# Kernel optimization log

Hardware: AMD Instinct MI355X
Metric: run time of the kernel (lower is better)

Reference implementation:

```python
import jax, jax.numpy as jnp
import numpy as np

N = 50000      # nodes
E = 800000     # edges (before self-loops)
F_IN = 256     # num_features
H = 8          # heads (conv1)
C = 32         # hidden_size per head (conv1)
OUT = 2        # conv2 out channels (1 head)
NEG_SLOPE = 0.2


def setup_inputs() -> dict:
    key = jax.random.key(0)
    ks = jax.random.split(key, 12)
    x = jax.random.normal(ks[0], (N, F_IN), jnp.float32)
    edge_index = jax.random.randint(ks[1], (2, E), 0, N, dtype=jnp.int64)

    def glorot(k, shape):
        fan = shape[0] if len(shape) == 2 else int(np.prod(shape))
        s = float(np.sqrt(6.0 / (fan + shape[-1])))
        return jax.random.uniform(k, shape, jnp.float32, -s, s)

    W1 = glorot(ks[2], (F_IN, H * C))
    att_src1 = glorot(ks[3], (H, C))
    att_dst1 = glorot(ks[4], (H, C))
    b1 = jnp.zeros((H * C,), jnp.float32)
    W2 = glorot(ks[5], (H * C, 1 * OUT))
    att_src2 = glorot(ks[6], (1, OUT))
    att_dst2 = glorot(ks[7], (1, OUT))
    b2 = jnp.zeros((OUT,), jnp.float32)
    return {"x": x, "edge_index": edge_index, "W1": W1, "att_src1": att_src1,
            "att_dst1": att_dst1, "b1": b1, "W2": W2, "att_src2": att_src2,
            "att_dst2": att_dst2, "b2": b2}


def gat_conv(x, src, dst, W, a_src, a_dst, b, heads, ch, n):
    # x: [n, f] -> projected [n, heads, ch]
    xp = (x @ W).reshape(n, heads, ch)
    alpha_src = jnp.einsum('nhc,hc->nh', xp, a_src)   # [n, H]
    alpha_dst = jnp.einsum('nhc,hc->nh', xp, a_dst)   # [n, H]
    e = jax.nn.leaky_relu(alpha_src[src] + alpha_dst[dst], NEG_SLOPE)  # [E', H]
    # segment softmax over edges grouped by destination node
    m = jax.ops.segment_max(e, dst, num_segments=n)                    # [n, H]
    p = jnp.exp(e - m[dst])
    denom = jax.ops.segment_sum(p, dst, num_segments=n)                # [n, H]
    alpha = p / denom[dst]                                             # [E', H]
    # weighted scatter-aggregate of source messages
    out = jax.ops.segment_sum(xp[src] * alpha[:, :, None], dst, num_segments=n)
    return out.reshape(n, heads * ch) + b


def reference(x, edge_index, W1, att_src1, att_dst1, b1, W2, att_src2, att_dst2, b2):
    n = x.shape[0]
    loops = jnp.arange(n, dtype=edge_index.dtype)  # GATConv add_self_loops=True
    src = jnp.concatenate([edge_index[0], loops])
    dst = jnp.concatenate([edge_index[1], loops])
    h = jax.nn.relu(gat_conv(x, src, dst, W1, att_src1, att_dst1, b1, H, C, n))
    # eval mode: F.dropout and attention dropout are identity
    return gat_conv(h, src, dst, W2, att_src2, att_dst2, b2, 1, OUT, n)
```

## Files before the change

kernel.cpp:

```cpp
#include <hip/hip_runtime.h>
#include <math.h>

#define N_NODES 50000
#define N_EDGES 800000
#define EP (N_EDGES + N_NODES)
#define NEG 0.2f
#define SCAN_BLOCKS 49
#define HB N_NODES

typedef __attribute__((ext_vector_type(8))) short bf16x8;
typedef __attribute__((ext_vector_type(4))) float f32x4;
typedef __attribute__((ext_vector_type(2))) float f32x2;

static __device__ __forceinline__ unsigned short bf16_rn(float f) {
    union { float f; unsigned int u; } v; v.f = f;
    unsigned int u = v.u;
    unsigned int r = (u + 0x7FFFu + ((u >> 16) & 1u)) >> 16;
    return (unsigned short)r;
}
static __device__ __forceinline__ f32x2 bf2_unpack(unsigned int u) {
    union { unsigned int i; float f; } a, b;
    a.i = u << 16; b.i = u & 0xFFFF0000u;
    return (f32x2){a.f, b.f};
}


__global__ void k_hist(const int* __restrict__ ei, int* __restrict__ counts) {
    int e = blockIdx.x * 256 + threadIdx.x;
    if (e >= EP) return;
    int d = (e < N_EDGES) ? ei[N_EDGES + e] : (e - N_EDGES);
    atomicAdd(&counts[d], 1);
}

__global__ void k_scan_block(const int* __restrict__ counts, int* __restrict__ excl,
                             int* __restrict__ bsums) {
    __shared__ int wsum[4];
    int b = blockIdx.x, t = threadIdx.x;
    int lane = t & 63, w = t >> 6;
    int i0 = b * 1024 + t * 4;
    int v0 = (i0 + 0 < N_NODES) ? counts[i0 + 0] : 0;
    int v1 = (i0 + 1 < N_NODES) ? counts[i0 + 1] : 0;
    int v2 = (i0 + 2 < N_NODES) ? counts[i0 + 2] : 0;
    int v3 = (i0 + 3 < N_NODES) ? counts[i0 + 3] : 0;
    int s = v0 + v1 + v2 + v3;
    int incl = s;
    #pragma unroll
    for (int d = 1; d < 64; d <<= 1) {
        int u = __shfl_up(incl, d);
        if (lane >= d) incl += u;
    }
    if (lane == 63) wsum[w] = incl;
    __syncthreads();
    if (t == 0) {
        int run = 0;
        #pragma unroll
        for (int i = 0; i < 4; ++i) { int x = wsum[i]; wsum[i] = run; run += x; }
        bsums[b] = run;
    }
    __syncthreads();
    int base = wsum[w] + incl - s;
    if (i0 + 0 < N_NODES) excl[i0 + 0] = base;
    if (i0 + 1 < N_NODES) excl[i0 + 1] = base + v0;
    if (i0 + 2 < N_NODES) excl[i0 + 2] = base + v0 + v1;
    if (i0 + 3 < N_NODES) excl[i0 + 3] = base + v0 + v1 + v2;
}

__global__ void k_scan_add(int* __restrict__ row_ptr, const int* __restrict__ bsums) {
    __shared__ int soff;
    int b = blockIdx.x, t = threadIdx.x;
    if (t < 64) {
        int v = (t < SCAN_BLOCKS) ? bsums[t] : 0;
        int incl = v;
        #pragma unroll
        for (int d = 1; d < 64; d <<= 1) {
            int u = __shfl_up(incl, d);
            if (t >= d) incl += u;
        }
        if (t == b) soff = incl - v;
    }
    __syncthreads();
    int off = soff;
    int i0 = b * 1024 + t * 4;
    #pragma unroll
    for (int j = 0; j < 4; ++j)
        if (i0 + j < N_NODES) row_ptr[i0 + j] += off;
    if (b == 0 && t == 0) row_ptr[N_NODES] = EP;
}

__global__ void k_scatter(const int* __restrict__ ei, const int* __restrict__ row_ptr,
                          int* __restrict__ fill, int* __restrict__ colb) {
    int e = blockIdx.x * 256 + threadIdx.x;
    if (e >= EP) return;
    int s, d;
    if (e < N_EDGES) { s = ei[e]; d = ei[N_EDGES + e]; }
    else             { s = e - N_EDGES; d = s; }
    int pos = row_ptr[d] + atomicAdd(&fill[d], 1);
    colb[pos] = s;
}

__global__ void k_cvtWfrag(const float* __restrict__ W1, bf16x8* __restrict__ Wfrag) {
    int ft = blockIdx.x * 256 + threadIdx.x;
    int c = ft >> 10, rem = ft & 1023;
    int nt = rem >> 6, l = rem & 63;
    int n = (l & 15) * 16 + nt;
    int k0 = c * 32 + (l >> 4) * 8;
    bf16x8 f;
    #pragma unroll
    for (int j = 0; j < 8; ++j)
        f[j] = (short)bf16_rn(W1[(k0 + j) * 256 + n]);
    Wfrag[ft] = f;
}

#define GM_GRID 782
__global__ __launch_bounds__(256) void
k_gemm1m(const float* __restrict__ x, const bf16x8* __restrict__ Wfrag,
         unsigned short* __restrict__ xph,
         const float* __restrict__ asrc, const float* __restrict__ adst,
         float* __restrict__ as1T, float* __restrict__ ad1T) {
    __shared__ bf16x8 lds[1024];
    int t = threadIdx.x, l = t & 63, w = t >> 6;
    int rowbase = blockIdx.x * 64 + w * 16;
    int m = l & 15, kg = l >> 4;

    f32x4 acc[16];
    #pragma unroll
    for (int nt = 0; nt < 16; ++nt)
        acc[nt] = (f32x4){0.f, 0.f, 0.f, 0.f};

    int r0 = rowbase + m;
    if (r0 > N_NODES - 1) r0 = N_NODES - 1;
    const float4* x4 = (const float4*)x;

    for (int c = 0; c < 8; ++c) {
        __syncthreads();
        const bf16x8* src = Wfrag + c * 1024;
        #pragma unroll
        for (int q = 0; q < 4; ++q)
            lds[q * 256 + t] = src[q * 256 + t];
        __syncthreads();

        int kb = (c * 32 + kg * 8) >> 2;
        float4 xa0 = x4[r0 * 64 + kb], xb0 = x4[r0 * 64 + kb + 1];
        bf16x8 aF0;
        aF0[0] = (short)bf16_rn(xa0.x); aF0[1] = (short)bf16_rn(xa0.y);
        aF0[2] = (short)bf16_rn(xa0.z); aF0[3] = (short)bf16_rn(xa0.w);
        aF0[4] = (short)bf16_rn(xb0.x); aF0[5] = (short)bf16_rn(xb0.y);
        aF0[6] = (short)bf16_rn(xb0.z); aF0[7] = (short)bf16_rn(xb0.w);

        #pragma unroll
        for (int nt = 0; nt < 16; ++nt) {
            bf16x8 bF = lds[nt * 64 + l];
            acc[nt] = __builtin_amdgcn_mfma_f32_16x16x32_bf16(aF0, bF, acc[nt], 0, 0, 0);
        }
    }

    int cbase = l & 15, rq = l >> 4;
    int head = cbase >> 1, hhalf = cbase & 1;
    float asV[16], adV[16];
    #pragma unroll
    for (int q = 0; q < 4; ++q) {
        float4 sa = ((const float4*)asrc)[cbase * 4 + q];
        float4 da = ((const float4*)adst)[cbase * 4 + q];
        asV[q * 4 + 0] = sa.x; asV[q * 4 + 1] = sa.y; asV[q * 4 + 2] = sa.z; asV[q * 4 + 3] = sa.w;
        adV[q * 4 + 0] = da.x; adV[q * 4 + 1] = da.y; adV[q * 4 + 2] = da.z; adV[q * 4 + 3] = da.w;
    }
    #pragma unroll
    for (int reg = 0; reg < 4; ++reg) {
        int gr = rowbase + rq * 4 + reg;
        unsigned int ob[8];
        float ps = 0.f, pd = 0.f;
        #pragma unroll
        for (int q = 0; q < 8; ++q) {
            float v0 = acc[2 * q][reg], v1 = acc[2 * q + 1][reg];
            ob[q] = (unsigned int)bf16_rn(v0) | ((unsigned int)bf16_rn(v1) << 16);
            ps = fmaf(v0, asV[2 * q], ps);     ps = fmaf(v1, asV[2 * q + 1], ps);
            pd = fmaf(v0, adV[2 * q], pd);     pd = fmaf(v1, adV[2 * q + 1], pd);
        }
        ps += __shfl_xor(ps, 1);
        pd += __shfl_xor(pd, 1);
        if (gr < N_NODES) {
            uint4* dst = (uint4*)(xph + (head * HB + gr) * 32 + hhalf * 16);
            dst[0] = make_uint4(ob[0], ob[1], ob[2], ob[3]);
            dst[1] = make_uint4(ob[4], ob[5], ob[6], ob[7]);
            if (hhalf == 0) {
                as1T[head * HB + gr] = ps;
                ad1T[head * HB + gr] = pd;
            }
        }
    }
}

#define AGH_GRID (782 * 8)
__global__ __launch_bounds__(256) void
k_aggh(const uint4* __restrict__ xph4, const float* __restrict__ as1T,
       const float* __restrict__ ad1T, const int* __restrict__ row_ptr,
       const int* __restrict__ colb, const float* __restrict__ b1,
       const float* __restrict__ W2, float2* __restrict__ hpart) {
    int t = threadIdx.x, l = t & 63, w = t >> 6;
    int bid = blockIdx.x;
    int h = bid & 7;
    int g = bid >> 3;
    int node = g * 64 + w * 16 + (l >> 2);
    int sub = l & 3;
    int qb = l & 60;
    bool alive = node < N_NODES;
    int nc = alive ? node : (N_NODES - 1);
    int start = row_ptr[nc], end = row_ptr[nc + 1];
    if (!alive) end = start;
    float adn = ad1T[h * HB + nc];
    const float* asb = as1T + h * HB;
    const uint4* xb = xph4 + (size_t)h * (HB * 4);

    f32x2 a0 = {0.f, 0.f}, a1 = {0.f, 0.f}, a2 = {0.f, 0.f}, a3 = {0.f, 0.f};
    float den = 0.f;

    int j = start;
    int s_pf = 0; float av_pf = 0.f; bool v_pf = false;
    if (j < end) {
        int jj = j + sub;
        v_pf = jj < end;
        s_pf = colb[v_pf ? jj : (end - 1)];
        av_pf = asb[s_pf];
    }
    while (j < end) {
        int s_cur = s_pf; float av_cur = av_pf; bool v_cur = v_pf;
        j += 4;
        if (j < end) {
            int jj = j + sub;
            v_pf = jj < end;
            s_pf = colb[v_pf ? jj : (end - 1)];
            av_pf = asb[s_pf];
        }
        float e = av_cur + adn;
        e = (e > 0.f) ? e : NEG * e;
        float p = v_cur ? __expf(e) : 0.f;
        den += p;
        #pragma unroll
        for (int eidx = 0; eidx < 4; ++eidx) {
            int   se = __shfl(s_cur, qb + eidx);
            float pe = __shfl(p,     qb + eidx);
            uint4 r = xb[(size_t)se * 4 + sub];
            f32x2 q = {pe, pe};
            a0 += q * bf2_unpack(r.x);
            a1 += q * bf2_unpack(r.y);
            a2 += q * bf2_unpack(r.z);
            a3 += q * bf2_unpack(r.w);
        }
    }
    den += __shfl_xor(den, 1);
    den += __shfl_xor(den, 2);

    float inv = 1.f / den;
    const float4* b4 = (const float4*)b1;
    float4 ba = b4[h * 8 + sub * 2 + 0];
    float4 bb = b4[h * 8 + sub * 2 + 1];
    float o0 = fmaxf(fmaf(a0[0], inv, ba.x), 0.f);
    float o1 = fmaxf(fmaf(a0[1], inv, ba.y), 0.f);
    float o2 = fmaxf(fmaf(a1[0], inv, ba.z), 0.f);
    float o3 = fmaxf(fmaf(a1[1], inv, ba.w), 0.f);
    float o4 = fmaxf(fmaf(a2[0], inv, bb.x), 0.f);
    float o5 = fmaxf(fmaf(a2[1], inv, bb.y), 0.f);
    float o6 = fmaxf(fmaf(a3[0], inv, bb.z), 0.f);
    float o7 = fmaxf(fmaf(a3[1], inv, bb.w), 0.f);
    const float4* W4 = (const float4*)W2;
    float4 wA = W4[h * 16 + sub * 4 + 0];
    float4 wB = W4[h * 16 + sub * 4 + 1];
    float4 wC = W4[h * 16 + sub * 4 + 2];
    float4 wD = W4[h * 16 + sub * 4 + 3];
    float d0 = o0 * wA.x + o1 * wA.z + o2 * wB.x + o3 * wB.z
             + o4 * wC.x + o5 * wC.z + o6 * wD.x + o7 * wD.z;
    float d1 = o0 * wA.y + o1 * wA.w + o2 * wB.y + o3 * wB.w
             + o4 * wC.y + o5 * wC.w + o6 * wD.y + o7 * wD.w;
    d0 += __shfl_xor(d0, 1);  d0 += __shfl_xor(d0, 2);
    d1 += __shfl_xor(d1, 1);  d1 += __shfl_xor(d1, 2);
    if (sub == 0 && alive)
        hpart[node * 8 + h] = (float2){d0, d1};
}

__global__ void k_post(const float2* __restrict__ hpart, const float* __restrict__ as2w,
                       const float* __restrict__ ad2w, float4* __restrict__ pk) {
    int n = blockIdx.x * 256 + threadIdx.x;
    if (n >= N_NODES) return;
    const float4* hp4 = (const float4*)(hpart + n * 8);
    float d0 = 0.f, d1 = 0.f;
    #pragma unroll
    for (int q = 0; q < 4; ++q) {
        float4 v = hp4[q];
        d0 += v.x + v.z;
        d1 += v.y + v.w;
    }
    float4 r;
    r.x = d0;
    r.y = d1;
    r.z = d0 * as2w[0] + d1 * as2w[1];
    r.w = d0 * ad2w[0] + d1 * ad2w[1];
    pk[n] = r;
}

__global__ void k_agg2(const float4* __restrict__ pk, const int* __restrict__ row_ptr,
                       const int* __restrict__ colb, const float* __restrict__ b2,
                       float* __restrict__ out) {
    int t = threadIdx.x;
    int g = t >> 4, lane = t & 15;
    int n = blockIdx.x * 16 + g;
    int start = row_ptr[n], end = row_ptr[n + 1];
    float adn = pk[n].w;
    float a0 = 0.f, a1 = 0.f, den = 0.f;
    for (int j = start + lane; j < end; j += 16) {
        int s = colb[j];
        float4 r = pk[s];
        float e = r.z + adn;
        e = (e > 0.f) ? e : NEG * e;
        float p = __expf(e);
        den += p;
        a0 = fmaf(p, r.x, a0);
        a1 = fmaf(p, r.y, a1);
    }
    #pragma unroll
    for (int m = 1; m < 16; m <<= 1) {
        a0 += __shfl_xor(a0, m);
        a1 += __shfl_xor(a1, m);
        den += __shfl_xor(den, m);
    }
    if (lane == 0) {
        out[2 * n] = a0 / den + b2[0];
        out[2 * n + 1] = a1 / den + b2[1];
    }
}

extern "C" void kernel_launch(void* const* d_in, const int* in_sizes, int n_in,
                              void* d_out, int out_size, void* d_ws, size_t ws_size,
                              hipStream_t stream) {
    const float* x     = (const float*)d_in[0];
    const int*   ei    = (const int*)d_in[1];
    const float* W1    = (const float*)d_in[2];
    const float* asrc1 = (const float*)d_in[3];
    const float* adst1 = (const float*)d_in[4];
    const float* b1    = (const float*)d_in[5];
    const float* W2    = (const float*)d_in[6];
    const float* asrc2 = (const float*)d_in[7];
    const float* adst2 = (const float*)d_in[8];
    const float* b2    = (const float*)d_in[9];
    float* out = (float*)d_out;

    char* ws = (char*)d_ws;
    unsigned short* xph = (unsigned short*)(ws + 0);
    bf16x8* Wfrag  = (bf16x8*)(ws + 25600000);
    float2* hpart  = (float2*)(ws + 25800000);
    float* as1T    = (float*)(ws + 102400000);
    float* ad1T    = (float*)(ws + 104000000);
    float4* pk     = (float4*)(ws + 105600000);
    int*   counts  = (int*)  (ws + 106400000);
    int*   fill    = (int*)  (ws + 106600000);
    int*   row_ptr = (int*)  (ws + 106800000);
    int*   colb    = (int*)  (ws + 107000064);
    int*   bsums   = (int*)  (ws + 110400064);

    hipMemsetAsync(counts, 0, 400000, stream);

    int egrid = (EP + 255) / 256;
    k_hist      <<<egrid,       256, 0, stream>>>(ei, counts);
    k_scan_block<<<SCAN_BLOCKS, 256, 0, stream>>>(counts, row_ptr, bsums);
    k_scan_add  <<<SCAN_BLOCKS, 256, 0, stream>>>(row_ptr, bsums);
    k_scatter   <<<egrid,       256, 0, stream>>>(ei, row_ptr, fill, colb);

    k_cvtWfrag  <<<32,     256, 0, stream>>>(W1, Wfrag);
    k_gemm1m   <<<GM_GRID, 256, 0, stream>>>(x, Wfrag, xph, asrc1, adst1, as1T, ad1T);
    k_aggh     <<<AGH_GRID, 256, 0, stream>>>((const uint4*)xph, as1T, ad1T, row_ptr, colb,
                                              b1, W2, hpart);
    k_post     <<<196,     256, 0, stream>>>(hpart, asrc2, adst2, pk);
    k_agg2     <<<3125,    256, 0, stream>>>(pk, row_ptr, colb, b2, out);
}
```

Baseline: 297.8 us.

## Precompute per-edge attention exponentials in scatter kernel, simplify aggregation loop

Moves the CSR scatter after the first GEMM and fuses into it the per-edge leaky-ReLU and exp for all 8 heads, storing them in CSR order as a [E',8] array. Attention scalars are now stored node-major so one edge reads 8 heads contiguously. The per-head aggregation kernel then reads the precomputed exponentials, so it no longer does a random as1T gather or exp per head, and it handles 8 edges per iteration without the software prefetch. The cost is an extra ~27MB write and read of the exponential array, and the scatter now runs after the GEMM, so it can no longer overlap with it.

```diff
diff --git a/kernel.cpp b/kernel.cpp
--- a/kernel.cpp
+++ b/kernel.cpp
@@ -22,6 +22,10 @@
     union { unsigned int i; float f; } a, b;
     a.i = u << 16; b.i = u & 0xFFFF0000u;
     return (f32x2){a.f, b.f};
+}
+static __device__ __forceinline__ float leaky_exp(float e) {
+    e = (e > 0.f) ? e : NEG * e;
+    return __expf(e);
 }
 
 
@@ -88,7 +92,9 @@
 }
 
 __global__ void k_scatter(const int* __restrict__ ei, const int* __restrict__ row_ptr,
-                          int* __restrict__ fill, int* __restrict__ colb) {
+                          int* __restrict__ fill, int* __restrict__ colb,
+                          const float* __restrict__ as1n, const float* __restrict__ ad1n,
+                          float* __restrict__ pst) {
     int e = blockIdx.x * 256 + threadIdx.x;
     if (e >= EP) return;
     int s, d;
@@ -96,6 +102,22 @@
     else             { s = e - N_EDGES; d = s; }
     int pos = row_ptr[d] + atomicAdd(&fill[d], 1);
     colb[pos] = s;
+    const float4* a4 = (const float4*)as1n;
+    const float4* d4 = (const float4*)ad1n;
+    float4 sa0 = a4[s * 2], sa1 = a4[s * 2 + 1];
+    float4 da0 = d4[d * 2], da1 = d4[d * 2 + 1];
+    float4 q0, q1;
+    q0.x = leaky_exp(sa0.x + da0.x);
+    q0.y = leaky_exp(sa0.y + da0.y);
+    q0.z = leaky_exp(sa0.z + da0.z);
+    q0.w = leaky_exp(sa0.w + da0.w);
+    q1.x = leaky_exp(sa1.x + da1.x);
+    q1.y = leaky_exp(sa1.y + da1.y);
+    q1.z = leaky_exp(sa1.z + da1.z);
+    q1.w = leaky_exp(sa1.w + da1.w);
+    float4* pp = (float4*)(pst + (size_t)pos * 8);
+    pp[0] = q0;
+    pp[1] = q1;
 }
 
 __global__ void k_cvtWfrag(const float* __restrict__ W1, bf16x8* __restrict__ Wfrag) {
@@ -116,7 +138,7 @@
 k_gemm1m(const float* __restrict__ x, const bf16x8* __restrict__ Wfrag,
          unsigned short* __restrict__ xph,
          const float* __restrict__ asrc, const float* __restrict__ adst,
-         float* __restrict__ as1T, float* __restrict__ ad1T) {
+         float* __restrict__ as1n, float* __restrict__ ad1n) {
     __shared__ bf16x8 lds[1024];
     int t = threadIdx.x, l = t & 63, w = t >> 6;
     int rowbase = blockIdx.x * 64 + w * 16;
@@ -183,8 +205,8 @@
             dst[0] = make_uint4(ob[0], ob[1], ob[2], ob[3]);
             dst[1] = make_uint4(ob[4], ob[5], ob[6], ob[7]);
             if (hhalf == 0) {
-                as1T[head * HB + gr] = ps;
-                ad1T[head * HB + gr] = pd;
+                as1n[gr * 8 + head] = ps;
+                ad1n[gr * 8 + head] = pd;
             }
         }
     }
@@ -192,10 +214,10 @@
 
 #define AGH_GRID (782 * 8)
 __global__ __launch_bounds__(256) void
-k_aggh(const uint4* __restrict__ xph4, const float* __restrict__ as1T,
-       const float* __restrict__ ad1T, const int* __restrict__ row_ptr,
-       const int* __restrict__ colb, const float* __restrict__ b1,
-       const float* __restrict__ W2, float2* __restrict__ hpart) {
+k_aggh(const uint4* __restrict__ xph4, const float* __restrict__ pst,
+       const int* __restrict__ row_ptr, const int* __restrict__ colb,
+       const float* __restrict__ b1, const float* __restrict__ W2,
+       float2* __restrict__ hpart) {
     int t = threadIdx.x, l = t & 63, w = t >> 6;
     int bid = blockIdx.x;
     int h = bid & 7;
@@ -207,44 +229,33 @@
     int nc = alive ? node : (N_NODES - 1);
     int start = row_ptr[nc], end = row_ptr[nc + 1];
     if (!alive) end = start;
-    float adn = ad1T[h * HB + nc];
-    const float* asb = as1T + h * HB;
     const uint4* xb = xph4 + (size_t)h * (HB * 4);
 
     f32x2 a0 = {0.f, 0.f}, a1 = {0.f, 0.f}, a2 = {0.f, 0.f}, a3 = {0.f, 0.f};
     float den = 0.f;
 
-    int j = start;
-    int s_pf = 0; float av_pf = 0.f; bool v_pf = false;
-    if (j < end) {
-        int jj = j + sub;
-        v_pf = jj < end;
-        s_pf = colb[v_pf ? jj : (end - 1)];
-        av_pf = asb[s_pf];
-    }
-    while (j < end) {
-        int s_cur = s_pf; float av_cur = av_pf; bool v_cur = v_pf;
-        j += 4;
-        if (j < end) {
-            int jj = j + sub;
-            v_pf = jj < end;
-            s_pf = colb[v_pf ? jj : (end - 1)];
-            av_pf = asb[s_pf];
-        }
-        float e = av_cur + adn;
-        e = (e > 0.f) ? e : NEG * e;
-        float p = v_cur ? __expf(e) : 0.f;
-        den += p;
-        #pragma unroll
-        for (int eidx = 0; eidx < 4; ++eidx) {
-            int   se = __shfl(s_cur, qb + eidx);
-            float pe = __shfl(p,     qb + eidx);
-            uint4 r = xb[(size_t)se * 4 + sub];
-            f32x2 q = {pe, pe};
-            a0 += q * bf2_unpack(r.x);
-            a1 += q * bf2_unpack(r.y);
-            a2 += q * bf2_unpack(r.z);
-            a3 += q * bf2_unpack(r.w);
+    for (int j = start; j < end; j += 8) {
+        int j0 = j + sub, j1 = j + 4 + sub;
+        bool v0 = j0 < end, v1 = j1 < end;
+        int s0 = colb[v0 ? j0 : start];
+        int s1 = colb[v1 ? j1 : start];
+        float p0 = v0 ? pst[(size_t)j0 * 8 + h] : 0.f;
+        float p1 = v1 ? pst[(size_t)j1 * 8 + h] : 0.f;
+        den += p0 + p1;
+        #pragma unroll
+        for (int e2 = 0; e2 < 8; ++e2) {
+            int   src = (e2 < 4) ? s0 : s1;
+            float pp  = (e2 < 4) ? p0 : p1;
+            int   se = __shfl(src, qb + (e2 & 3));
+            float pe = __shfl(pp,  qb + (e2 & 3));
+            if (j + e2 < end) {
+                uint4 r = xb[(size_t)se * 4 + sub];
+                f32x2 q = {pe, pe};
+                a0 += q * bf2_unpack(r.x);
+                a1 += q * bf2_unpack(r.y);
+                a2 += q * bf2_unpack(r.z);
+                a3 += q * bf2_unpack(r.w);
+            }
         }
     }
     den += __shfl_xor(den, 1);
@@ -347,8 +358,9 @@
     unsigned short* xph = (unsigned short*)(ws + 0);
     bf16x8* Wfrag  = (bf16x8*)(ws + 25600000);
     float2* hpart  = (float2*)(ws + 25800000);
-    float* as1T    = (float*)(ws + 102400000);
-    float* ad1T    = (float*)(ws + 104000000);
+    float* pst     = (float*)(ws + 29000000);
+    float* as1n    = (float*)(ws + 102400000);
+    float* ad1n    = (float*)(ws + 104000000);
     float4* pk     = (float4*)(ws + 105600000);
     int*   counts  = (int*)  (ws + 106400000);
     int*   fill    = (int*)  (ws + 106600000);
@@ -362,11 +374,11 @@
     k_hist      <<<egrid,       256, 0, stream>>>(ei, counts);
     k_scan_block<<<SCAN_BLOCKS, 256, 0, stream>>>(counts, row_ptr, bsums);
     k_scan_add  <<<SCAN_BLOCKS, 256, 0, stream>>>(row_ptr, bsums);
-    k_scatter   <<<egrid,       256, 0, stream>>>(ei, row_ptr, fill, colb);
 
     k_cvtWfrag  <<<32,     256, 0, stream>>>(W1, Wfrag);
-    k_gemm1m   <<<GM_GRID, 256, 0, stream>>>(x, Wfrag, xph, asrc1, adst1, as1T, ad1T);
-    k_aggh     <<<AGH_GRID, 256, 0, stream>>>((const uint4*)xph, as1T, ad1T, row_ptr, colb,
+    k_gemm1m   <<<GM_GRID, 256, 0, stream>>>(x, Wfrag, xph, asrc1, adst1, as1n, ad1n);
+    k_scatter   <<<egrid,   256, 0, stream>>>(ei, row_ptr, fill, colb, as1n, ad1n, pst);
+    k_aggh     <<<AGH_GRID, 256, 0, stream>>>((const uint4*)xph, pst, row_ptr, colb,
                                               b1, W2, hpart);
     k_post     <<<196,     256, 0, stream>>>(hpart, asrc2, adst2, pk);
     k_agg2     <<<3125,    256, 0, stream>>>(pk, row_ptr, colb, b2, out);
```

Result: slower. 334.8 us (+12.4%).
